# Kernel optimization log

Measured on AMD Instinct MI355X. Metric: run time of the kernel, lower is better.

Reference implementation:

```python
import jax, jax.numpy as jnp
import numpy as np

N_NODES = 10000
N_EDGES = 160000
N_TYPES = 128          # rows in SymbolicEmbeddingsVQ table
N_SYMBOLS = 64
PATTERN_LEN = 8
SYMBOL_DIM = 16
HIDDEN = PATTERN_LEN * SYMBOL_DIM  # mode='concat' -> 128
NUM_RADIAL = 6


def setup_inputs() -> dict:
    key = jax.random.key(0)
    ks = jax.random.split(key, 10)
    x = jax.random.randint(ks[0], (N_NODES,), 0, N_TYPES)
    rbf = jax.random.normal(ks[1], (N_EDGES, NUM_RADIAL), dtype=jnp.float32)
    i = jax.random.randint(ks[2], (N_EDGES,), 0, N_NODES)
    j = jax.random.randint(ks[3], (N_EDGES,), 0, N_NODES)
    # VQ symbolic embedding params: each of 128 types is a pattern of
    # PATTERN_LEN symbol ids; symbols are vectors from a codebook.
    code_idx = jax.random.randint(ks[4], (N_TYPES, PATTERN_LEN), 0, N_SYMBOLS)
    codebook = jax.random.normal(ks[5], (N_SYMBOLS, SYMBOL_DIM), dtype=jnp.float32)
    # Linear layers (PyTorch Linear default uniform init approximated by scaled normals)
    W_rbf = jax.random.normal(ks[6], (NUM_RADIAL, HIDDEN), dtype=jnp.float32) / np.sqrt(NUM_RADIAL)
    b_rbf = jnp.zeros((HIDDEN,), dtype=jnp.float32)
    W = jax.random.normal(ks[7], (3 * HIDDEN, HIDDEN), dtype=jnp.float32) / np.sqrt(3 * HIDDEN)
    b = jnp.zeros((HIDDEN,), dtype=jnp.float32)
    return {"x": x, "rbf": rbf, "i": i, "j": j, "code_idx": code_idx,
            "codebook": codebook, "W_rbf": W_rbf, "b_rbf": b_rbf, "W": W, "b": b}


def reference(x, rbf, i, j, code_idx, codebook, W_rbf, b_rbf, W, b):
    act = jax.nn.silu
    # Symbolic VQ embedding, mode='concat': table[t] = concat of PATTERN_LEN codebook vectors
    table = codebook[code_idx].reshape(N_TYPES, HIDDEN)   # [128, hidden]
    h = table[x]                                          # [N_nodes, hidden]
    r = act(rbf @ W_rbf + b_rbf)                          # [E, hidden]
    feat = jnp.concatenate([h[i], h[j], r], axis=-1)      # [E, 3*hidden]
    return act(feat @ W + b)                              # [E, hidden]
```

## Files before the change

### kernel.cpp

```cpp
#include <hip/hip_runtime.h>
#include <hip/hip_bf16.h>
#include <stdint.h>

typedef __attribute__((ext_vector_type(8))) short bf16x8;
typedef __attribute__((ext_vector_type(4))) float f32x4;
typedef __attribute__((ext_vector_type(4))) unsigned short u16x4;

__device__ __forceinline__ float silu_f(float x) {
    return x * __builtin_amdgcn_rcpf(1.0f + __expf(-x));
}

__device__ __forceinline__ unsigned short f2bf(float x) {
    union { float f; unsigned int u; } v; v.f = x;
    unsigned int r = v.u + 0x7fffu + ((v.u >> 16) & 1u);
    return (unsigned short)(r >> 16);
}
__device__ __forceinline__ float bf2f(unsigned short u) {
    union { unsigned int u; float f; } v; v.u = ((unsigned int)u) << 16;
    return v.f;
}

__device__ __forceinline__ void async16(void* l, const void* g) {
    auto lds3 = (__attribute__((address_space(3))) unsigned int*)(uintptr_t)l;
    auto g1   = (const __attribute__((address_space(1))) unsigned int*)(uintptr_t)g;
    __builtin_amdgcn_global_load_lds(g1, lds3, 16, 0, 0);
}

__global__ void prep_P(const int* __restrict__ code_idx,
                       const float* __restrict__ codebook,
                       const float* __restrict__ W,
                       const float* __restrict__ b,
                       unsigned short* __restrict__ P1,
                       unsigned short* __restrict__ P2,
                       unsigned short* __restrict__ Wt3)
{
    __shared__ float trow[128];
    const int t = blockIdx.x, tid = threadIdx.x;
    if (tid < 128) {
        int sym = code_idx[t * 8 + (tid >> 4)];
        trow[tid] = codebook[sym * 16 + (tid & 15)];
    } else {
        int k = tid - 128;
        Wt3[t * 128 + k] = f2bf(W[(256 + k) * 128 + t]);
    }
    __syncthreads();
    const int which = tid >> 7, o = tid & 127;
    const float* Wb = W + which * 16384;
    float acc = which ? 0.0f : b[o];
#pragma unroll 8
    for (int k = 0; k < 128; ++k)
        acc += trow[k] * Wb[k * 128 + o];
    (which ? P2 : P1)[t * 128 + o] = f2bf(acc);
}

__global__ __launch_bounds__(512, 6) void fused_main(
    const int* __restrict__ x,
    const float* __restrict__ rbf,
    const int* __restrict__ ei,
    const int* __restrict__ ej,
    const float* __restrict__ W_rbf,
    const float* __restrict__ b_rbf,
    const unsigned short* __restrict__ P1,
    const unsigned short* __restrict__ P2,
    const unsigned short* __restrict__ Wt3,
    float* __restrict__ out)
{
    __shared__ __align__(16) unsigned char lB[32768];
    __shared__ __align__(16) unsigned char lA[16384];
    __shared__ __align__(16) unsigned char lR[1536];

    const int tid  = threadIdx.x;
    const int lane = tid & 63;
    const int w    = tid >> 6;
    const int e0   = blockIdx.x * 64;

    const int quad = lane >> 4, l15 = lane & 15, l7 = l15 & 7;
    const int wm = (w >> 1) * 16;
    const int wn = (w & 1) * 64;

    {
        const int ri = lane >> 4, ch = lane & 15;
#pragma unroll
        for (int rr = 0; rr < 4; ++rr) {
            int g = w * 4 + rr;
            int o = g * 4 + ri;
            int jc = ch ^ (o & 7);
            async16(lB + g * 1024, Wt3 + o * 128 + jc * 8);
        }
    }
    if (w == 0)
        async16(lR, (const unsigned char*)rbf + (size_t)e0 * 24 + lane * 16);
    else if (w == 1 && lane < 32)
        async16(lR + 1024, (const unsigned char*)rbf + (size_t)e0 * 24 + 1024 + lane * 16);

    int ti, tj;
    {
        int e = e0 + wm + l15;
        ti = x[ei[e]];
        tj = x[ej[e]];
    }

    const int j16 = tid & 15, gg = tid >> 4, cb = j16 * 8;
    float wr[6][8], br[8];
#pragma unroll
    for (int q = 0; q < 6; ++q) {
        const float4* p = (const float4*)(W_rbf + q * 128 + cb);
        float4 a = p[0], c = p[1];
        wr[q][0]=a.x; wr[q][1]=a.y; wr[q][2]=a.z; wr[q][3]=a.w;
        wr[q][4]=c.x; wr[q][5]=c.y; wr[q][6]=c.z; wr[q][7]=c.w;
    }
    {
        const float4* p = (const float4*)(b_rbf + cb);
        float4 a = p[0], c = p[1];
        br[0]=a.x; br[1]=a.y; br[2]=a.z; br[3]=a.w;
        br[4]=c.x; br[5]=c.y; br[6]=c.z; br[7]=c.w;
    }

    __syncthreads();

#pragma unroll
    for (int i = 0; i < 2; ++i) {
        int m = gg * 2 + i;
        const float* rr_ = (const float*)(lR + m * 24);
        float f0 = rr_[0], f1 = rr_[1], f2 = rr_[2],
              f3 = rr_[3], f4 = rr_[4], f5 = rr_[5];
        bf16x8 pk;
#pragma unroll
        for (int c = 0; c < 8; ++c) {
            float a = br[c] + f0*wr[0][c] + f1*wr[1][c] + f2*wr[2][c]
                            + f3*wr[3][c] + f4*wr[4][c] + f5*wr[5][c];
            pk[c] = (short)f2bf(silu_f(a));
        }
        int p = j16 ^ (m & 7);
        *(bf16x8*)(lA + m * 256 + p * 16) = pk;
    }

    u16x4 q1[4], q2[4];
#pragma unroll
    for (int ni = 0; ni < 4; ++ni) {
        int o = wn + ni * 16 + quad * 4;
        q1[ni] = *(const u16x4*)(P1 + ti * 128 + o);
        q2[ni] = *(const u16x4*)(P2 + tj * 128 + o);
    }

    __syncthreads();

    bf16x8 Bf[4][4];
#pragma unroll
    for (int ni = 0; ni < 4; ++ni) {
        const unsigned char* brow = lB + (wn + ni * 16 + l15) * 256;
#pragma unroll
        for (int ks = 0; ks < 4; ++ks)
            Bf[ni][ks] = *(const bf16x8*)(brow + (((ks * 4 + quad) ^ l7) * 16));
    }
    bf16x8 af[4];
    {
        const unsigned char* arow = lA + (wm + l15) * 256;
#pragma unroll
        for (int ks = 0; ks < 4; ++ks)
            af[ks] = *(const bf16x8*)(arow + (((ks * 4 + quad) ^ l7) * 16));
    }

    f32x4 acc[4] = {};
#pragma unroll
    for (int ks = 0; ks < 4; ++ks)
#pragma unroll
        for (int ni = 0; ni < 4; ++ni)
            acc[ni] = __builtin_amdgcn_mfma_f32_16x16x32_bf16(
                Bf[ni][ks], af[ks], acc[ni], 0, 0, 0);

    {
        size_t e = (size_t)(e0 + wm + l15);
        float* orow = out + e * 128 + wn;
#pragma unroll
        for (int ni = 0; ni < 4; ++ni) {
            f32x4 v;
#pragma unroll
            for (int r = 0; r < 4; ++r)
                v[r] = silu_f(acc[ni][r] + bf2f(q1[ni][r]) + bf2f(q2[ni][r]));
            *(f32x4*)(orow + ni * 16 + quad * 4) = v;
        }
    }
}

extern "C" void kernel_launch(void* const* d_in, const int* in_sizes, int n_in,
                              void* d_out, int out_size, void* d_ws, size_t ws_size,
                              hipStream_t stream) {
    const int*   x        = (const int*)d_in[0];
    const float* rbf      = (const float*)d_in[1];
    const int*   ei       = (const int*)d_in[2];
    const int*   ej       = (const int*)d_in[3];
    const int*   code_idx = (const int*)d_in[4];
    const float* codebook = (const float*)d_in[5];
    const float* W_rbf    = (const float*)d_in[6];
    const float* b_rbf    = (const float*)d_in[7];
    const float* W        = (const float*)d_in[8];
    const float* b        = (const float*)d_in[9];
    float* out = (float*)d_out;

    const int nE = in_sizes[2];

    if (ws_size < 98304) return;
    unsigned short* P1  = (unsigned short*)d_ws;
    unsigned short* P2  = P1 + 16384;
    unsigned short* Wt3 = P2 + 16384;

    prep_P<<<128, 256, 0, stream>>>(code_idx, codebook, W, b, P1, P2, Wt3);
    fused_main<<<nE / 64, 512, 0, stream>>>(x, rbf, ei, ej, W_rbf, b_rbf,
                                            P1, P2, Wt3, out);
}
```

Measured before the change: 152.8 us.

## Compute per-wave rbf A-tile rows to drop block barrier before MFMA

Each wave now computes the silu(rbf@W_rbf) bf16 rows for its own 16-edge slice and writes them to LDS. It then waits only on its own LDS writes (lgkmcnt) instead of a second block-wide __syncthreads. The node-type index loads are issued earlier, before the async weight copies, to start the dependent gather sooner. The A and B fragments are now loaded per k-step rather than all up front, which lowers register pressure. In exchange, the two waves sharing a row slice both compute the same rbf rows, doubling that small piece of ALU work.

After: 159.2 us. 1.04x slower.

```diff
diff --git a/kernel.cpp b/kernel.cpp
--- a/kernel.cpp
+++ b/kernel.cpp
@@ -5,6 +5,7 @@
 typedef __attribute__((ext_vector_type(8))) short bf16x8;
 typedef __attribute__((ext_vector_type(4))) float f32x4;
 typedef __attribute__((ext_vector_type(4))) unsigned short u16x4;
+typedef __attribute__((ext_vector_type(2))) unsigned int u32x2;
 
 __device__ __forceinline__ float silu_f(float x) {
     return x * __builtin_amdgcn_rcpf(1.0f + __expf(-x));
@@ -78,6 +79,13 @@
     const int wm = (w >> 1) * 16;
     const int wn = (w & 1) * 64;
 
+    int ti, tj;
+    {
+        int e = e0 + wm + l15;
+        ti = x[ei[e]];
+        tj = x[ej[e]];
+    }
+
     {
         const int ri = lane >> 4, ch = lane & 15;
 #pragma unroll
@@ -93,47 +101,12 @@
     else if (w == 1 && lane < 32)
         async16(lR + 1024, (const unsigned char*)rbf + (size_t)e0 * 24 + 1024 + lane * 16);
 
-    int ti, tj;
-    {
-        int e = e0 + wm + l15;
-        ti = x[ei[e]];
-        tj = x[ej[e]];
-    }
-
-    const int j16 = tid & 15, gg = tid >> 4, cb = j16 * 8;
-    float wr[6][8], br[8];
-#pragma unroll
-    for (int q = 0; q < 6; ++q) {
-        const float4* p = (const float4*)(W_rbf + q * 128 + cb);
-        float4 a = p[0], c = p[1];
-        wr[q][0]=a.x; wr[q][1]=a.y; wr[q][2]=a.z; wr[q][3]=a.w;
-        wr[q][4]=c.x; wr[q][5]=c.y; wr[q][6]=c.z; wr[q][7]=c.w;
-    }
-    {
-        const float4* p = (const float4*)(b_rbf + cb);
-        float4 a = p[0], c = p[1];
-        br[0]=a.x; br[1]=a.y; br[2]=a.z; br[3]=a.w;
-        br[4]=c.x; br[5]=c.y; br[6]=c.z; br[7]=c.w;
-    }
-
-    __syncthreads();
-
-#pragma unroll
-    for (int i = 0; i < 2; ++i) {
-        int m = gg * 2 + i;
-        const float* rr_ = (const float*)(lR + m * 24);
-        float f0 = rr_[0], f1 = rr_[1], f2 = rr_[2],
-              f3 = rr_[3], f4 = rr_[4], f5 = rr_[5];
-        bf16x8 pk;
-#pragma unroll
-        for (int c = 0; c < 8; ++c) {
-            float a = br[c] + f0*wr[0][c] + f1*wr[1][c] + f2*wr[2][c]
-                            + f3*wr[3][c] + f4*wr[4][c] + f5*wr[5][c];
-            pk[c] = (short)f2bf(silu_f(a));
-        }
-        int p = j16 ^ (m & 7);
-        *(bf16x8*)(lA + m * 256 + p * 16) = pk;
-    }
+    const int cb4 = lane >> 1, h = lane & 1;
+    float4 wr[6], br;
+#pragma unroll
+    for (int q = 0; q < 6; ++q)
+        wr[q] = *(const float4*)(W_rbf + q * 128 + cb4 * 4);
+    br = *(const float4*)(b_rbf + cb4 * 4);
 
     u16x4 q1[4], q2[4];
 #pragma unroll
@@ -145,29 +118,47 @@
 
     __syncthreads();
 
-    bf16x8 Bf[4][4];
-#pragma unroll
-    for (int ni = 0; ni < 4; ++ni) {
-        const unsigned char* brow = lB + (wn + ni * 16 + l15) * 256;
-#pragma unroll
-        for (int ks = 0; ks < 4; ++ks)
-            Bf[ni][ks] = *(const bf16x8*)(brow + (((ks * 4 + quad) ^ l7) * 16));
-    }
-    bf16x8 af[4];
-    {
-        const unsigned char* arow = lA + (wm + l15) * 256;
-#pragma unroll
-        for (int ks = 0; ks < 4; ++ks)
-            af[ks] = *(const bf16x8*)(arow + (((ks * 4 + quad) ^ l7) * 16));
-    }
+    const int ch16 = cb4 >> 1, halfoff = (cb4 & 1) * 8;
+#pragma unroll
+    for (int i = 0; i < 8; ++i) {
+        int m = wm + h * 8 + i;
+        const float* rr_ = (const float*)(lR + m * 24);
+        float f0 = rr_[0], f1 = rr_[1], f2 = rr_[2],
+              f3 = rr_[3], f4 = rr_[4], f5 = rr_[5];
+        float a0 = br.x + f0*wr[0].x + f1*wr[1].x + f2*wr[2].x
+                        + f3*wr[3].x + f4*wr[4].x + f5*wr[5].x;
+        float a1 = br.y + f0*wr[0].y + f1*wr[1].y + f2*wr[2].y
+                        + f3*wr[3].y + f4*wr[4].y + f5*wr[5].y;
+        float a2 = br.z + f0*wr[0].z + f1*wr[1].z + f2*wr[2].z
+                        + f3*wr[3].z + f4*wr[4].z + f5*wr[5].z;
+        float a3 = br.w + f0*wr[0].w + f1*wr[1].w + f2*wr[2].w
+                        + f3*wr[3].w + f4*wr[4].w + f5*wr[5].w;
+        unsigned int lo = (unsigned int)f2bf(silu_f(a0))
+                        | ((unsigned int)f2bf(silu_f(a1)) << 16);
+        unsigned int hi = (unsigned int)f2bf(silu_f(a2))
+                        | ((unsigned int)f2bf(silu_f(a3)) << 16);
+        int p = ch16 ^ (m & 7);
+        u32x2 pk; pk[0] = lo; pk[1] = hi;
+        *(u32x2*)(lA + m * 256 + p * 16 + halfoff) = pk;
+    }
+
+    asm volatile("s_waitcnt lgkmcnt(0)" ::: "memory");
+    __builtin_amdgcn_sched_barrier(0);
 
     f32x4 acc[4] = {};
 #pragma unroll
-    for (int ks = 0; ks < 4; ++ks)
+    for (int ks = 0; ks < 4; ++ks) {
+        const int p = (ks * 4 + quad) ^ l7;
+        bf16x8 af = *(const bf16x8*)(lA + (wm + l15) * 256 + p * 16);
+        bf16x8 bfv[4];
+#pragma unroll
+        for (int ni = 0; ni < 4; ++ni)
+            bfv[ni] = *(const bf16x8*)(lB + (wn + ni * 16 + l15) * 256 + p * 16);
 #pragma unroll
         for (int ni = 0; ni < 4; ++ni)
             acc[ni] = __builtin_amdgcn_mfma_f32_16x16x32_bf16(
-                Bf[ni][ks], af[ks], acc[ni], 0, 0, 0);
+                bfv[ni], af, acc[ni], 0, 0, 0);
+    }
 
     {
         size_t e = (size_t)(e0 + wm + l15);
```
